# Optimization experiments

Measured on AMD Instinct MI355X. Metric: run time of the kernel, lower is better.

The kernel has to match this reference:

```python
import jax, jax.numpy as jnp
import numpy as np

D_MODEL = 1024
N_HEADS = 16
HEAD_DIM = D_MODEL // N_HEADS


def setup_inputs() -> dict:
    key = jax.random.key(0)
    ks = jax.random.split(key, 5)
    scale = 1.0 / np.sqrt(D_MODEL)
    x = jax.random.normal(ks[0], (2, 2048, D_MODEL), dtype=jnp.float32)
    Wq = jax.random.normal(ks[1], (D_MODEL, D_MODEL), dtype=jnp.float32) * scale
    Wk = jax.random.normal(ks[2], (D_MODEL, D_MODEL), dtype=jnp.float32) * scale
    Wv = jax.random.normal(ks[3], (D_MODEL, D_MODEL), dtype=jnp.float32) * scale
    Wo = jax.random.normal(ks[4], (D_MODEL, D_MODEL), dtype=jnp.float32) * scale
    return {"x": x, "Wq": Wq, "Wk": Wk, "Wv": Wv, "Wo": Wo}


def reference(x, Wq, Wk, Wv, Wo):
    # x: [B, S, D]; weights stored as [out, in] like nn.Linear -> y = x @ W.T
    B, S, D = x.shape
    H, Hd = N_HEADS, HEAD_DIM
    attn_scale = 1.0 / np.sqrt(Hd)

    def split_heads(t):  # [B,S,D] -> [B,H,S,Hd]
        return t.reshape(B, S, H, Hd).transpose(0, 2, 1, 3)

    q = split_heads(x @ Wq.T)
    k = split_heads(x @ Wk.T)
    v = split_heads(x @ Wv.T)

    scores = jnp.einsum('bhqd,bhkd->bhqk', q, k) * attn_scale  # [B,H,S,S]
    causal = jnp.tril(jnp.ones((S, S), dtype=bool))
    scores = jnp.where(causal, scores, jnp.finfo(scores.dtype).min)
    attn = jax.nn.softmax(scores, axis=-1)
    out = jnp.einsum('bhqk,bhkd->bhqd', attn, v)  # [B,H,S,Hd]
    out = out.transpose(0, 2, 1, 3).reshape(B, S, D)
    return out @ Wo.T
```

## Files before the change

kernel.cpp:

```cpp
#include <hip/hip_runtime.h>
#include <hip/hip_bf16.h>

typedef __attribute__((ext_vector_type(8))) __bf16 bf16x8;
typedef __attribute__((ext_vector_type(4))) __bf16 bf16x4;
typedef __attribute__((ext_vector_type(4))) float f32x4;

#define D_MODEL 1024
#define S_LEN   2048
#define BATCH   2
#define NH      16
#define HD      64
#define MROWS   (BATCH * S_LEN)

#define EXP2F(x) __builtin_amdgcn_exp2f(x)

__global__ __launch_bounds__(256) void cvt_bf16(const float* __restrict__ in,
                                                __bf16* __restrict__ out, int n4) {
    int i = blockIdx.x * 256 + threadIdx.x;
    if (i < n4) {
        float4 v = ((const float4*)in)[i];
        bf16x4 o = {(__bf16)v.x, (__bf16)v.y, (__bf16)v.z, (__bf16)v.w};
        ((bf16x4*)out)[i] = o;
    }
}

__global__ __launch_bounds__(256) void cvt_all(const float* __restrict__ x,
                                               const float* __restrict__ Wq,
                                               const float* __restrict__ Wk,
                                               const float* __restrict__ Wv,
                                               __bf16* __restrict__ xb,
                                               __bf16* __restrict__ wqkv) {
    const int nx = (MROWS * D_MODEL) / 4;
    const int nw = (D_MODEL * D_MODEL) / 4;
    int i = blockIdx.x * 256 + threadIdx.x;
    const float* src;
    __bf16* dst;
    int si, di;
    if (i < nx) {
        src = x; si = i; dst = xb; di = i;
    } else {
        int k = i - nx;
        int sel = k / nw;
        si = k - sel * nw;
        src = (sel == 0) ? Wq : (sel == 1) ? Wk : Wv;
        dst = wqkv; di = k;
    }
    float4 v = ((const float4*)src)[si];
    bf16x4 o = {(__bf16)v.x, (__bf16)v.y, (__bf16)v.z, (__bf16)v.w};
    ((bf16x4*)dst)[di] = o;
}

__device__ __forceinline__ void g2l16(const void* g, __bf16* l) {
    __builtin_amdgcn_global_load_lds((const __attribute__((address_space(1))) void*)g,
                                     (__attribute__((address_space(3))) void*)l, 16, 0, 0);
}

__global__ __launch_bounds__(256) void gemm_qkv(const __bf16* __restrict__ A,
                                                const __bf16* __restrict__ W,
                                                __bf16* __restrict__ Qb,
                                                __bf16* __restrict__ Kq,
                                                __bf16* __restrict__ VTb,
                                                float qs) {
    __shared__ __bf16 sa[128 * 64];
    __shared__ __bf16 sb[128 * 64];

    const int t    = threadIdx.x;
    const int lane = t & 63;
    const int wid  = t >> 6;
    const int lr   = lane & 15;
    const int lg   = lane >> 4;
    const int wr   = wid >> 1;
    const int wc   = wid & 1;
    const int K    = D_MODEL;
    const int m0   = blockIdx.y * 128;
    const int n0   = blockIdx.x * 128;

    const __bf16* Ab = A + (size_t)m0 * K;
    const __bf16* Wb = W + (size_t)n0 * K;

    f32x4 acc[4][4];
#pragma unroll
    for (int m = 0; m < 4; m++)
#pragma unroll
        for (int n = 0; n < 4; n++) acc[m][n] = (f32x4){0.f, 0.f, 0.f, 0.f};

    for (int k0 = 0; k0 < K; k0 += 64) {
#pragma unroll
        for (int i = 0; i < 4; i++) {
            int ca = i * 256 + t;
            int row = ca >> 3;
            int sc  = ((ca & 7) ^ (row & 7)) * 8;
            g2l16(&Ab[(size_t)row * K + k0 + sc], &sa[ca * 8]);
            g2l16(&Wb[(size_t)row * K + k0 + sc], &sb[ca * 8]);
        }
        __syncthreads();

        bf16x8 af[4][2], bfr[4][2];
#pragma unroll
        for (int m = 0; m < 4; m++) {
            const int row = wr * 64 + m * 16 + lr;
#pragma unroll
            for (int kc = 0; kc < 2; kc++)
                af[m][kc] = *(const bf16x8*)&sa[row * 64 + (((kc * 4 + lg) ^ (lr & 7)) * 8)];
        }
#pragma unroll
        for (int n = 0; n < 4; n++) {
            const int row = wc * 64 + n * 16 + lr;
#pragma unroll
            for (int kc = 0; kc < 2; kc++)
                bfr[n][kc] = *(const bf16x8*)&sb[row * 64 + (((kc * 4 + lg) ^ (lr & 7)) * 8)];
        }
#pragma unroll
        for (int m = 0; m < 4; m++)
#pragma unroll
            for (int n = 0; n < 4; n++)
#pragma unroll
                for (int kc = 0; kc < 2; kc++)
                    acc[m][n] = __builtin_amdgcn_mfma_f32_16x16x32_bf16(af[m][kc], bfr[n][kc], acc[m][n], 0, 0, 0);
        __syncthreads();
    }

#pragma unroll
    for (int m = 0; m < 4; m++) {
#pragma unroll
        for (int n = 0; n < 4; n++) {
#pragma unroll
            for (int j = 0; j < 4; j++) {
                int row = m0 + wr * 64 + m * 16 + lg * 4 + j;
                int col = n0 + wc * 64 + n * 16 + lr;
                float v = acc[m][n][j];
                if (col < 1024) {
                    Qb[(size_t)row * D_MODEL + col] = (__bf16)(v * qs);
                } else if (col < 2048) {
                    Kq[(size_t)row * D_MODEL + col - 1024] = (__bf16)v;
                } else {
                    int c2 = col - 2048;
                    int b = row >> 11, s = row & 2047;
                    int h = c2 >> 6, d = c2 & 63;
                    VTb[(((size_t)(b * NH + h) * HD + d) << 11) + s] = (__bf16)v;
                }
            }
        }
    }
}

__global__ __launch_bounds__(256) void gemm_out(const __bf16* __restrict__ A,
                                                const __bf16* __restrict__ W,
                                                float* __restrict__ C,
                                                int M, int N, int K) {
    __shared__ __bf16 sa[128 * 64];
    __shared__ __bf16 sb[64 * 64];

    const int t    = threadIdx.x;
    const int lane = t & 63;
    const int wid  = t >> 6;
    const int lr   = lane & 15;
    const int lg   = lane >> 4;
    const int wr   = wid >> 1;
    const int wc   = wid & 1;
    const int m0   = blockIdx.y * 128;
    const int n0   = blockIdx.x * 64;

    const __bf16* Ab = A + (size_t)m0 * K;
    const __bf16* Wb = W + (size_t)n0 * K;

    f32x4 acc[4][2];
#pragma unroll
    for (int m = 0; m < 4; m++)
#pragma unroll
        for (int n = 0; n < 2; n++) acc[m][n] = (f32x4){0.f, 0.f, 0.f, 0.f};

    for (int k0 = 0; k0 < K; k0 += 64) {
#pragma unroll
        for (int i = 0; i < 4; i++) {
            int ca = i * 256 + t;
            int row = ca >> 3;
            int sc  = ((ca & 7) ^ (row & 7)) * 8;
            g2l16(&Ab[(size_t)row * K + k0 + sc], &sa[ca * 8]);
        }
#pragma unroll
        for (int i = 0; i < 2; i++) {
            int ca = i * 256 + t;
            int row = ca >> 3;
            int sc  = ((ca & 7) ^ (row & 7)) * 8;
            g2l16(&Wb[(size_t)row * K + k0 + sc], &sb[ca * 8]);
        }
        __syncthreads();

        bf16x8 af[4][2], bfr[2][2];
#pragma unroll
        for (int m = 0; m < 4; m++) {
            const int row = wr * 64 + m * 16 + lr;
#pragma unroll
            for (int kc = 0; kc < 2; kc++)
                af[m][kc] = *(const bf16x8*)&sa[row * 64 + (((kc * 4 + lg) ^ (lr & 7)) * 8)];
        }
#pragma unroll
        for (int n = 0; n < 2; n++) {
            const int row = wc * 32 + n * 16 + lr;
#pragma unroll
            for (int kc = 0; kc < 2; kc++)
                bfr[n][kc] = *(const bf16x8*)&sb[row * 64 + (((kc * 4 + lg) ^ (lr & 7)) * 8)];
        }
#pragma unroll
        for (int m = 0; m < 4; m++)
#pragma unroll
            for (int n = 0; n < 2; n++)
#pragma unroll
                for (int kc = 0; kc < 2; kc++)
                    acc[m][n] = __builtin_amdgcn_mfma_f32_16x16x32_bf16(af[m][kc], bfr[n][kc], acc[m][n], 0, 0, 0);
        __syncthreads();
    }

#pragma unroll
    for (int m = 0; m < 4; m++)
#pragma unroll
        for (int n = 0; n < 2; n++)
#pragma unroll
            for (int j = 0; j < 4; j++) {
                int row = m0 + wr * 64 + m * 16 + lg * 4 + j;
                int col = n0 + wc * 32 + n * 16 + lr;
                C[(size_t)row * N + col] = acc[m][n][j];
            }
}

__global__ __launch_bounds__(256) void attn_fwd(const __bf16* __restrict__ Q,
                                                const __bf16* __restrict__ Kb,
                                                const __bf16* __restrict__ VT,
                                                __bf16* __restrict__ O) {
    __shared__ __bf16 kt[2][64 * 64];
    __shared__ __bf16 vt[2][64 * 64];
    __shared__ __bf16 pt[4][16][64];

    const int t    = threadIdx.x;
    const int lane = t & 63;
    const int wid  = t >> 6;
    const int lr   = lane & 15;
    const int lg   = lane >> 4;
    const int bid  = blockIdx.x;
    const int qb   = 31 - (bid >> 5);
    const int bh   = bid & 31;
    const int b    = bh >> 4;
    const int h    = bh & 15;
    const int col  = h * HD;

    const size_t qrow = (size_t)b * S_LEN + qb * 64 + wid * 16;
    const int qg = qb * 64 + wid * 16 + lr;
    const __bf16* Kbase = Kb + (size_t)b * S_LEN * D_MODEL + col;
    const __bf16* Vbase = VT + (size_t)bh * HD * S_LEN;
    const int pswz = (lr & 7) * 8;

    const int ca0 = t, ca1 = t + 256;
    const int r0 = ca0 >> 3, s0 = ((ca0 & 7) ^ (r0 & 7)) * 8;
    const int r1 = ca1 >> 3, s1 = ((ca1 & 7) ^ (r1 & 7)) * 8;

    bf16x8 qf[2];
#pragma unroll
    for (int c = 0; c < 2; c++)
        qf[c] = *(const bf16x8*)&Q[(qrow + lr) * D_MODEL + col + c * 32 + lg * 8];

    f32x4 o[4];
#pragma unroll
    for (int n = 0; n < 4; n++) o[n] = (f32x4){0.f, 0.f, 0.f, 0.f};
    float psum = 0.f;

    g2l16(&Kbase[(size_t)r0 * D_MODEL + s0], &kt[0][ca0 * 8]);
    g2l16(&Kbase[(size_t)r1 * D_MODEL + s1], &kt[0][ca1 * 8]);
    g2l16(&Vbase[(size_t)r0 * S_LEN + s0],   &vt[0][ca0 * 8]);
    g2l16(&Vbase[(size_t)r1 * S_LEN + s1],   &vt[0][ca1 * 8]);
    __syncthreads();

    for (int kvt = 0; kvt <= qb; kvt++) {
        const int kv0 = kvt * 64;
        const int cur = kvt & 1;
        const bool diag = (kvt == qb);

        if (kvt < qb) {
            const int nb = cur ^ 1;
            const int kv1 = kv0 + 64;
            g2l16(&Kbase[(size_t)(kv1 + r0) * D_MODEL + s0], &kt[nb][ca0 * 8]);
            g2l16(&Kbase[(size_t)(kv1 + r1) * D_MODEL + s1], &kt[nb][ca1 * 8]);
            g2l16(&Vbase[(size_t)r0 * S_LEN + kv1 + s0],     &vt[nb][ca0 * 8]);
            g2l16(&Vbase[(size_t)r1 * S_LEN + kv1 + s1],     &vt[nb][ca1 * 8]);
        }

        f32x4 s[4];
        __builtin_amdgcn_s_setprio(1);
#pragma unroll
        for (int tt = 0; tt < 4; tt++) {
            s[tt] = (f32x4){0.f, 0.f, 0.f, 0.f};
#pragma unroll
            for (int c = 0; c < 2; c++) {
                const int row = tt * 16 + lr;
                bf16x8 kf = *(const bf16x8*)&kt[cur][row * 64 + (((c * 4 + lg) ^ (lr & 7)) * 8)];
                s[tt] = __builtin_amdgcn_mfma_f32_16x16x32_bf16(kf, qf[c], s[tt], 0, 0, 0);
            }
        }
        __builtin_amdgcn_s_setprio(0);

        if (diag) {
#pragma unroll
            for (int tt = 0; tt < 4; tt++) {
                int kg = kv0 + tt * 16 + lg * 4;
#pragma unroll
                for (int j = 0; j < 4; j++)
                    if (kg + j > qg) s[tt][j] = -1e30f;
            }
        }

#pragma unroll
        for (int tt = 0; tt < 4; tt++) {
            float p0 = EXP2F(s[tt][0]), p1 = EXP2F(s[tt][1]);
            float p2 = EXP2F(s[tt][2]), p3 = EXP2F(s[tt][3]);
            psum += (p0 + p1) + (p2 + p3);
            bf16x4 pw = {(__bf16)p0, (__bf16)p1, (__bf16)p2, (__bf16)p3};
            *(bf16x4*)&pt[wid][lr][(tt * 16 + lg * 4) ^ pswz] = pw;
        }

        asm volatile("s_waitcnt lgkmcnt(0)" ::: "memory");
        __builtin_amdgcn_sched_barrier(0);

        __builtin_amdgcn_s_setprio(1);
#pragma unroll
        for (int c = 0; c < 2; c++) {
            bf16x8 pa = *(const bf16x8*)&pt[wid][lr][(c * 32 + lg * 8) ^ pswz];
#pragma unroll
            for (int n = 0; n < 4; n++) {
                const int d = n * 16 + lr;
                bf16x8 vf = *(const bf16x8*)&vt[cur][d * 64 + (((c * 4 + lg) ^ (lr & 7)) * 8)];
                o[n] = __builtin_amdgcn_mfma_f32_16x16x32_bf16(pa, vf, o[n], 0, 0, 0);
            }
        }
        __builtin_amdgcn_s_setprio(0);

        __syncthreads();
    }

    psum += __shfl_xor(psum, 16, 64);
    psum += __shfl_xor(psum, 32, 64);
    float inv = 1.0f / psum;
    float invj[4];
#pragma unroll
    for (int j = 0; j < 4; j++) invj[j] = __shfl(inv, lg * 4 + j, 64);

#pragma unroll
    for (int n = 0; n < 4; n++) {
#pragma unroll
        for (int j = 0; j < 4; j++) {
            float val = o[n][j] * invj[j];
            O[(qrow + lg * 4 + j) * D_MODEL + col + n * 16 + lr] = (__bf16)val;
        }
    }
}

extern "C" void kernel_launch(void* const* d_in, const int* in_sizes, int n_in,
                              void* d_out, int out_size, void* d_ws, size_t ws_size,
                              hipStream_t stream) {
    const float* x  = (const float*)d_in[0];
    const float* Wq = (const float*)d_in[1];
    const float* Wk = (const float*)d_in[2];
    const float* Wv = (const float*)d_in[3];
    const float* Wo = (const float*)d_in[4];
    float* out = (float*)d_out;

    const size_t XE = (size_t)MROWS * D_MODEL;
    const size_t WE = (size_t)D_MODEL * D_MODEL;
    __bf16* xb  = (__bf16*)d_ws;
    __bf16* Qb  = xb + XE;
    __bf16* Kq  = Qb + XE;
    __bf16* VTb = Kq + XE;
    __bf16* AO  = xb;

    __bf16* wqkv = (__bf16*)d_out;
    __bf16* wob  = Qb;

    const int ncv = (int)(XE / 4 + 3 * WE / 4);
    cvt_all<<<(ncv + 255) / 256, 256, 0, stream>>>(x, Wq, Wk, Wv, xb, wqkv);

    const float qs = 0.125f * 1.44269504088896340736f;
    gemm_qkv<<<dim3(3 * D_MODEL / 128, MROWS / 128), 256, 0, stream>>>(xb, wqkv, Qb, Kq, VTb, qs);

    attn_fwd<<<1024, 256, 0, stream>>>(Qb, Kq, VTb, AO);

    cvt_bf16<<<(int)(WE / 4 / 256), 256, 0, stream>>>(Wo, wob, (int)(WE / 4));
    gemm_out<<<dim3(D_MODEL / 64, MROWS / 128), 256, 0, stream>>>(AO, wob, out, MROWS, D_MODEL, D_MODEL);
}
```

Measured before the change: 113.9 us.

## Double-buffer LDS in projection GEMMs and narrow QKV GEMM tile to 64 columns

Both the QKV and output-projection GEMMs now use two LDS buffers. The next K-slice is issued with global_load_lds while MFMAs run on the current slice, which leaves one barrier per iteration instead of two. The QKV GEMM tile also shrinks from 128x128 to 128x64, doubling the grid to 1536 blocks so more CUs are busy. The trade-off is more LDS per block and less operand reuse per block in the QKV GEMM.

```diff
diff --git a/kernel.cpp b/kernel.cpp
--- a/kernel.cpp
+++ b/kernel.cpp
@@ -61,8 +61,8 @@
                                                 __bf16* __restrict__ Kq,
                                                 __bf16* __restrict__ VTb,
                                                 float qs) {
-    __shared__ __bf16 sa[128 * 64];
-    __shared__ __bf16 sb[128 * 64];
+    __shared__ __bf16 sa[2][128 * 64];
+    __shared__ __bf16 sb[2][64 * 64];
 
     const int t    = threadIdx.x;
     const int lane = t & 63;
@@ -73,61 +73,75 @@
     const int wc   = wid & 1;
     const int K    = D_MODEL;
     const int m0   = blockIdx.y * 128;
-    const int n0   = blockIdx.x * 128;
+    const int n0   = blockIdx.x * 64;
 
     const __bf16* Ab = A + (size_t)m0 * K;
     const __bf16* Wb = W + (size_t)n0 * K;
 
-    f32x4 acc[4][4];
+    f32x4 acc[4][2];
 #pragma unroll
     for (int m = 0; m < 4; m++)
 #pragma unroll
-        for (int n = 0; n < 4; n++) acc[m][n] = (f32x4){0.f, 0.f, 0.f, 0.f};
-
-    for (int k0 = 0; k0 < K; k0 += 64) {
+        for (int n = 0; n < 2; n++) acc[m][n] = (f32x4){0.f, 0.f, 0.f, 0.f};
+
+    auto stage = [&](int buf, int k0) {
 #pragma unroll
         for (int i = 0; i < 4; i++) {
             int ca = i * 256 + t;
             int row = ca >> 3;
             int sc  = ((ca & 7) ^ (row & 7)) * 8;
-            g2l16(&Ab[(size_t)row * K + k0 + sc], &sa[ca * 8]);
-            g2l16(&Wb[(size_t)row * K + k0 + sc], &sb[ca * 8]);
-        }
-        __syncthreads();
-
-        bf16x8 af[4][2], bfr[4][2];
+            g2l16(&Ab[(size_t)row * K + k0 + sc], &sa[buf][ca * 8]);
+        }
+#pragma unroll
+        for (int i = 0; i < 2; i++) {
+            int ca = i * 256 + t;
+            int row = ca >> 3;
+            int sc  = ((ca & 7) ^ (row & 7)) * 8;
+            g2l16(&Wb[(size_t)row * K + k0 + sc], &sb[buf][ca * 8]);
+        }
+    };
+
+    stage(0, 0);
+    __syncthreads();
+
+    for (int k0 = 0; k0 < K; k0 += 64) {
+        const int cur = (k0 >> 6) & 1;
+        if (k0 + 64 < K) stage(cur ^ 1, k0 + 64);
+
+        bf16x8 af[4][2], bfr[2][2];
 #pragma unroll
         for (int m = 0; m < 4; m++) {
             const int row = wr * 64 + m * 16 + lr;
 #pragma unroll
             for (int kc = 0; kc < 2; kc++)
-                af[m][kc] = *(const bf16x8*)&sa[row * 64 + (((kc * 4 + lg) ^ (lr & 7)) * 8)];
-        }
-#pragma unroll
-        for (int n = 0; n < 4; n++) {
-            const int row = wc * 64 + n * 16 + lr;
+                af[m][kc] = *(const bf16x8*)&sa[cur][row * 64 + (((kc * 4 + lg) ^ (lr & 7)) * 8)];
+        }
+#pragma unroll
+        for (int n = 0; n < 2; n++) {
+            const int row = wc * 32 + n * 16 + lr;
 #pragma unroll
             for (int kc = 0; kc < 2; kc++)
-                bfr[n][kc] = *(const bf16x8*)&sb[row * 64 + (((kc * 4 + lg) ^ (lr & 7)) * 8)];
+                bfr[n][kc] = *(const bf16x8*)&sb[cur][row * 64 + (((kc * 4 + lg) ^ (lr & 7)) * 8)];
         }
 #pragma unroll
         for (int m = 0; m < 4; m++)
 #pragma unroll
-            for (int n = 0; n < 4; n++)
+            for (int n = 0; n < 2; n++)
 #pragma unroll
                 for (int kc = 0; kc < 2; kc++)
                     acc[m][n] = __builtin_amdgcn_mfma_f32_16x16x32_bf16(af[m][kc], bfr[n][kc], acc[m][n], 0, 0, 0);
+
         __syncthreads();
     }
 
 #pragma unroll
     for (int m = 0; m < 4; m++) {
 #pragma unroll
-        for (int n = 0; n < 4; n++) {
+        for (int n = 0; n < 2; n++) {
 #pragma unroll
             for (int j = 0; j < 4; j++) {
                 int row = m0 + wr * 64 + m * 16 + lg * 4 + j;
-                int col = n0 + wc * 64 + n * 16 + lr;
+                int col = n0 + wc * 32 + n * 16 + lr;
                 float v = acc[m][n][j];
                 if (col < 1024) {
                     Qb[(size_t)row * D_MODEL + col] = (__bf16)(v * qs);
@@ -148,8 +162,8 @@
                                                 const __bf16* __restrict__ W,
                                                 float* __restrict__ C,
                                                 int M, int N, int K) {
-    __shared__ __bf16 sa[128 * 64];
-    __shared__ __bf16 sb[64 * 64];
+    __shared__ __bf16 sa[2][128 * 64];
+    __shared__ __bf16 sb[2][64 * 64];
 
     const int t    = threadIdx.x;
     const int lane = t & 63;
@@ -170,22 +184,29 @@
 #pragma unroll
         for (int n = 0; n < 2; n++) acc[m][n] = (f32x4){0.f, 0.f, 0.f, 0.f};
 
-    for (int k0 = 0; k0 < K; k0 += 64) {
+    auto stage = [&](int buf, int k0) {
 #pragma unroll
         for (int i = 0; i < 4; i++) {
             int ca = i * 256 + t;
             int row = ca >> 3;
             int sc  = ((ca & 7) ^ (row & 7)) * 8;
-            g2l16(&Ab[(size_t)row * K + k0 + sc], &sa[ca * 8]);
+            g2l16(&Ab[(size_t)row * K + k0 + sc], &sa[buf][ca * 8]);
         }
 #pragma unroll
         for (int i = 0; i < 2; i++) {
             int ca = i * 256 + t;
             int row = ca >> 3;
             int sc  = ((ca & 7) ^ (row & 7)) * 8;
-            g2l16(&Wb[(size_t)row * K + k0 + sc], &sb[ca * 8]);
-        }
-        __syncthreads();
+            g2l16(&Wb[(size_t)row * K + k0 + sc], &sb[buf][ca * 8]);
+        }
+    };
+
+    stage(0, 0);
+    __syncthreads();
+
+    for (int k0 = 0; k0 < K; k0 += 64) {
+        const int cur = (k0 >> 6) & 1;
+        if (k0 + 64 < K) stage(cur ^ 1, k0 + 64);
 
         bf16x8 af[4][2], bfr[2][2];
 #pragma unroll
@@ -193,14 +214,14 @@
             const int row = wr * 64 + m * 16 + lr;
 #pragma unroll
             for (int kc = 0; kc < 2; kc++)
-                af[m][kc] = *(const bf16x8*)&sa[row * 64 + (((kc * 4 + lg) ^ (lr & 7)) * 8)];
+                af[m][kc] = *(const bf16x8*)&sa[cur][row * 64 + (((kc * 4 + lg) ^ (lr & 7)) * 8)];
         }
 #pragma unroll
         for (int n = 0; n < 2; n++) {
             const int row = wc * 32 + n * 16 + lr;
 #pragma unroll
             for (int kc = 0; kc < 2; kc++)
-                bfr[n][kc] = *(const bf16x8*)&sb[row * 64 + (((kc * 4 + lg) ^ (lr & 7)) * 8)];
+                bfr[n][kc] = *(const bf16x8*)&sb[cur][row * 64 + (((kc * 4 + lg) ^ (lr & 7)) * 8)];
         }
 #pragma unroll
         for (int m = 0; m < 4; m++)
@@ -209,6 +230,7 @@
 #pragma unroll
                 for (int kc = 0; kc < 2; kc++)
                     acc[m][n] = __builtin_amdgcn_mfma_f32_16x16x32_bf16(af[m][kc], bfr[n][kc], acc[m][n], 0, 0, 0);
+
         __syncthreads();
     }
 
@@ -378,7 +400,7 @@
     cvt_all<<<(ncv + 255) / 256, 256, 0, stream>>>(x, Wq, Wk, Wv, xb, wqkv);
 
     const float qs = 0.125f * 1.44269504088896340736f;
-    gemm_qkv<<<dim3(3 * D_MODEL / 128, MROWS / 128), 256, 0, stream>>>(xb, wqkv, Qb, Kq, VTb, qs);
+    gemm_qkv<<<dim3(3 * D_MODEL / 64, MROWS / 128), 256, 0, stream>>>(xb, wqkv, Qb, Kq, VTb, qs);
 
     attn_fwd<<<1024, 256, 0, stream>>>(Qb, Kq, VTb, AO);
 
```

Result: slower. 116.5 us (+2.3%).
